# Optimization experiments

Hardware: AMD Instinct MI355X
Metric: run time of the kernel (lower is better)

The kernel has to match this reference:

```python
import jax, jax.numpy as jnp
import numpy as np
import math

B, N, M, H = 4, 1024, 1024, 512
EPS = 1e-5


def _ln(x, g, b):
    m = jnp.mean(x, axis=-1, keepdims=True)
    v = jnp.mean((x - m) ** 2, axis=-1, keepdims=True)
    return (x - m) * jax.lax.rsqrt(v + EPS) * g + b


def _heads(x, h):
    b, s, Hh = x.shape
    return x.reshape(b, s, h, Hh // h).transpose(0, 2, 1, 3)  # [b,h,s,d]


def _merge(x):
    b, h, s, d = x.shape
    return x.transpose(0, 2, 1, 3).reshape(b, s, h * d)


def _sdpa(q, k, v):
    d = q.shape[-1]
    a = jax.nn.softmax(jnp.einsum('bhqd,bhkd->bhqk', q, k) / math.sqrt(d), axis=-1)
    return jnp.einsum('bhqk,bhkd->bhqd', a, v)


def _attn(key, value, query, Wk, Wv, Wq, Wf, bf, g, b, h):
    residual = query
    K = _heads(key @ Wk, h)
    V = _heads(value @ Wv, h)
    Q = _heads(query @ Wq, h)
    r = _merge(_sdpa(Q, K, V))
    r = jnp.concatenate([residual, r], axis=-1) @ Wf + bf
    return _ln(r + residual, g, b)


def _sc_attn(x, x2, Wk, Wv, Wq, Wf, bf, g, b, h=2):
    residual = x
    sK, sV, sQ = _heads(x @ Wk, h), _heads(x @ Wv, h), _heads(x @ Wq, h)
    cK, cV, cQ = _heads(x2 @ Wk, h), _heads(x2 @ Wv, h), _heads(x2 @ Wq, h)
    r = _sdpa(sQ, sK, sV) + _sdpa(cQ, cK, cV) + _sdpa(cQ, sK, sV) + _sdpa(sQ, cK, cV)
    r = _merge(r)
    r = jnp.concatenate([residual, r], axis=-1) @ Wf + bf
    return _ln(r + residual, g, b)


def _forward(context_x, context_y, target_x, in_W, in_b, cx_W, cx_b, tx_W, tx_b,
             sc_Wk, sc_Wv, sc_Wq, sc_Wf, sc_bf, sc_g, sc_b,
             ca_Wk, ca_Wv, ca_Wq, ca_Wf, ca_bf, ca_g, ca_b):
    bsz = context_x.shape[0]
    y = context_y.reshape(bsz, -1, 4, 2)
    proj = lambda yd: jnp.concatenate([context_x, yd], axis=-1) @ in_W + in_b
    e = proj(y[:, :, 0, :])
    e1 = proj(y[:, :, 1, :])
    e2 = proj(y[:, :, 2, :])
    e3 = proj(y[:, :, 3, :])
    # first self pass: key2/value2/query2 == current encoder_input
    for i in range(2):
        e = _sc_attn(e, e, sc_Wk[i], sc_Wv[i], sc_Wq[i], sc_Wf[i], sc_bf[i], sc_g[i], sc_b[i])
    for x2 in (e1, e2, e3):
        for i in range(2):
            e = _sc_attn(e, x2, sc_Wk[i], sc_Wv[i], sc_Wq[i], sc_Wf[i], sc_bf[i], sc_g[i], sc_b[i])
    q = target_x @ tx_W + tx_b
    k = context_x @ cx_W + cx_b
    for i in range(2):
        q = _attn(k, e, q, ca_Wk[i], ca_Wv[i], ca_Wq[i], ca_Wf[i], ca_bf[i], ca_g[i], ca_b[i], h=4)
    return q


def setup_inputs() -> dict:
    key = jax.random.key(0)
    ks = jax.random.split(key, 24)
    w = lambda i, shape, s: jax.random.normal(ks[i], shape, jnp.float32) * s
    return {
        'context_x': jax.random.normal(ks[0], (B, N, 1), jnp.float32),
        'context_y': jax.random.normal(ks[1], (B, N, 8), jnp.float32),
        'target_x': jax.random.normal(ks[2], (B, M, 1), jnp.float32),
        'in_W': w(3, (3, H), 0.5), 'in_b': jnp.zeros((H,), jnp.float32),
        'cx_W': w(4, (1, H), 0.5), 'cx_b': jnp.zeros((H,), jnp.float32),
        'tx_W': w(5, (1, H), 0.5), 'tx_b': jnp.zeros((H,), jnp.float32),
        'sc_Wk': w(6, (2, H, H), 0.03), 'sc_Wv': w(7, (2, H, H), 0.03), 'sc_Wq': w(8, (2, H, H), 0.03),
        'sc_Wf': w(9, (2, 2 * H, H), 0.03), 'sc_bf': jnp.zeros((2, H), jnp.float32),
        'sc_g': jnp.ones((2, H), jnp.float32), 'sc_b': jnp.zeros((2, H), jnp.float32),
        'ca_Wk': w(10, (2, H, H), 0.03), 'ca_Wv': w(11, (2, H, H), 0.03), 'ca_Wq': w(12, (2, H, H), 0.03),
        'ca_Wf': w(13, (2, 2 * H, H), 0.03), 'ca_bf': jnp.zeros((2, H), jnp.float32),
        'ca_g': jnp.ones((2, H), jnp.float32), 'ca_b': jnp.zeros((2, H), jnp.float32),
    }


def reference(context_x, context_y, target_x, in_W, in_b, cx_W, cx_b, tx_W, tx_b,
              sc_Wk, sc_Wv, sc_Wq, sc_Wf, sc_bf, sc_g, sc_b,
              ca_Wk, ca_Wv, ca_Wq, ca_Wf, ca_bf, ca_g, ca_b):
    return _forward(context_x, context_y, target_x, in_W, in_b, cx_W, cx_b, tx_W, tx_b,
                    sc_Wk, sc_Wv, sc_Wq, sc_Wf, sc_bf, sc_g, sc_b,
                    ca_Wk, ca_Wv, ca_Wq, ca_Wf, ca_bf, ca_g, ca_b)
```

## Files before the change

kernel.cpp:

```cpp
#include <hip/hip_runtime.h>

#define DEVINL __device__ __forceinline__

typedef short bf16x8 __attribute__((ext_vector_type(8)));
typedef float f32x4 __attribute__((ext_vector_type(4)));

DEVINL unsigned f2b(float f) {
  unsigned u = __float_as_uint(f);
  u = (u + 0x7FFFu + ((u >> 16) & 1u)) >> 16;
  return u & 0xFFFFu;
}
DEVINL uint4 pack8(const float* v) {
  uint4 u;
  u.x = f2b(v[0]) | (f2b(v[1]) << 16);
  u.y = f2b(v[2]) | (f2b(v[3]) << 16);
  u.z = f2b(v[4]) | (f2b(v[5]) << 16);
  u.w = f2b(v[6]) | (f2b(v[7]) << 16);
  return u;
}

DEVINL float4 block_sum4(float4 v, float4* sh) {
  const int lane = threadIdx.x & 63, wid = threadIdx.x >> 6;
#pragma unroll
  for (int o = 32; o; o >>= 1) {
    v.x += __shfl_down(v.x, o);
    v.y += __shfl_down(v.y, o);
    v.z += __shfl_down(v.z, o);
    v.w += __shfl_down(v.w, o);
  }
  __syncthreads();
  if (lane == 0) sh[wid] = v;
  __syncthreads();
  float4 a = sh[0], b = sh[1], c = sh[2], d = sh[3], r;
  r.x = a.x + b.x + c.x + d.x;
  r.y = a.y + b.y + c.y + d.y;
  r.z = a.z + b.z + c.z + d.z;
  r.w = a.w + b.w + c.w + d.w;
  return r;
}
DEVINL float block_sum1(float v, float* sh) {
  const int lane = threadIdx.x & 63, wid = threadIdx.x >> 6;
#pragma unroll
  for (int o = 32; o; o >>= 1) v += __shfl_down(v, o);
  __syncthreads();
  if (lane == 0) sh[wid] = v;
  __syncthreads();
  return sh[0] + sh[1] + sh[2] + sh[3];
}

__global__ __launch_bounds__(256) void tabproj_kernel(
    const float* __restrict__ V, const float* __restrict__ bias,
    const float* __restrict__ W, float* __restrict__ P, int nvec, float scl) {
  __shared__ float4 sh4[4];
  const int j = blockIdx.x, tid = threadIdx.x;
  float acc[4] = {0.f, 0.f, 0.f, 0.f};
  for (int kk = tid; kk < 512; kk += 256) {
    const float w = W[(size_t)kk * 512 + j];
    for (int v = 0; v < nvec; ++v) acc[v] += V[(size_t)v * 512 + kk] * w;
    acc[3] += bias[kk] * w;
  }
  float4 packed = make_float4(acc[0], acc[1], acc[2], acc[3]);
  packed = block_sum4(packed, sh4);
  if (tid == 0) {
    const float vals[4] = {packed.x * scl, packed.y * scl, packed.z * scl, packed.w * scl};
    for (int v = 0; v < nvec; ++v) P[(size_t)v * 512 + j] = vals[v];
    P[(size_t)nvec * 512 + j] = vals[3];
  }
}

__global__ __launch_bounds__(256) void transpose_bf_kernel(
    const float* __restrict__ src, unsigned short* __restrict__ dst, int K, int N,
    float scl) {
  __shared__ float tile[32][33];
  const int n0 = blockIdx.x * 32, k0 = blockIdx.y * 32;
  const int tx = threadIdx.x, ty = threadIdx.y;
#pragma unroll
  for (int r = 0; r < 4; ++r)
    tile[ty + 8 * r][tx] = src[(size_t)(k0 + ty + 8 * r) * N + n0 + tx];
  __syncthreads();
#pragma unroll
  for (int r = 0; r < 4; ++r)
    dst[(size_t)(n0 + ty + 8 * r) * K + k0 + tx] =
        (unsigned short)f2b(scl * tile[tx][ty + 8 * r]);
}

__global__ __launch_bounds__(256) void vtrans_frag_kernel(
    const float* __restrict__ V, int ld, int nh, int D,
    unsigned short* __restrict__ Vfr) {
  __shared__ float tile[32][33];
  const int s0 = blockIdx.x * 32, d0 = blockIdx.y * 32;
  const int bh = blockIdx.z;
  const int b = bh / nh, h = bh % nh;
  const int tx = threadIdx.x, ty = threadIdx.y;
  const float* src = V + ((size_t)b * 1024 + s0) * ld + h * D + d0;
#pragma unroll
  for (int r = 0; r < 4; ++r)
    tile[ty + 8 * r][tx] = src[(size_t)(ty + 8 * r) * ld + tx];
  __syncthreads();
  const int idx = ty * 32 + tx;
  if (idx < 128) {
    const int dj = idx & 31, sch = idx >> 5;
    float v[8];
#pragma unroll
    for (int jj = 0; jj < 8; ++jj) v[jj] = tile[sch * 8 + jj][dj];
    const uint4 u = pack8(v);
    const int sc = s0 >> 5;
    const int dtile = (d0 + dj) >> 4;
    const int lane = sch * 16 + (dj & 15);
    *(uint4*)(Vfr + ((size_t)(bh * 32 + sc) * (D / 16) + dtile) * 512 + lane * 8) = u;
  }
}

__global__ __launch_bounds__(256) void affine3_pack_kernel(
    const float* __restrict__ cx, const float* __restrict__ cy, int sel,
    const float* __restrict__ TK, const float* __restrict__ TV,
    const float* __restrict__ TQ, unsigned short* __restrict__ Kfr,
    unsigned short* __restrict__ Qbf, float* __restrict__ Vf) {
  const int row = blockIdx.x;
  const int b = row >> 10, s = row & 1023;
  const float x = cx[row];
  const float* y = cy + (size_t)row * 8 + 2 * sel;
  const float y0 = y[0], y1 = y[1];
  const int t = threadIdx.x;
  if (t < 128) {
    const bool isQ = t >= 64;
    const int c = t & 63;
    const int h = c >> 5;
    const int d0 = (c & 31) * 8;
    const float* T = isQ ? TQ : TK;
    float v[8];
#pragma unroll
    for (int j = 0; j < 8; ++j) {
      const int col = h * 256 + d0 + j;
      v[j] = x * T[col] + y0 * T[512 + col] + y1 * T[1024 + col] + T[1536 + col];
    }
    const uint4 u = pack8(v);
    const int bh = b * 2 + h;
    if (isQ) {
      *(uint4*)(Qbf + ((size_t)bh * 1024 + s) * 256 + d0) = u;
    } else {
      const int kc = d0 >> 5;
      const int lane = ((d0 & 31) >> 3) * 16 + (s & 15);
      *(uint4*)(Kfr + ((size_t)(bh * 8 + kc) * 64 + (s >> 4)) * 512 + lane * 8) = u;
    }
  } else {
    const int col0 = (t - 128) * 4;
    float4 o;
    float* op = (float*)&o;
#pragma unroll
    for (int j = 0; j < 4; ++j) {
      const int col = col0 + j;
      op[j] = x * TV[col] + y0 * TV[512 + col] + y1 * TV[1024 + col] + TV[1536 + col];
    }
    *(float4*)(Vf + (size_t)row * 512 + col0) = o;
  }
}

__global__ __launch_bounds__(64) void rank1_pack_kernel(
    const float* __restrict__ x, const float* __restrict__ T,
    unsigned short* __restrict__ dst, int isQ) {
  const int row = blockIdx.x;
  const int b = row >> 10, s = row & 1023;
  const float xv = x[row];
  const int c = threadIdx.x;
  const int h = c >> 4;
  const int d0 = (c & 15) * 8;
  float v[8];
#pragma unroll
  for (int j = 0; j < 8; ++j) {
    const int col = h * 128 + d0 + j;
    v[j] = xv * T[col] + T[512 + col];
  }
  const uint4 u = pack8(v);
  const int bh = b * 4 + h;
  if (isQ) {
    *(uint4*)(dst + ((size_t)bh * 1024 + s) * 128 + d0) = u;
  } else {
    const int kc = d0 >> 5;
    const int lane = ((d0 & 31) >> 3) * 16 + (s & 15);
    *(uint4*)(dst + ((size_t)(bh * 4 + kc) * 64 + (s >> 4)) * 512 + lane * 8) = u;
  }
}

__global__ __launch_bounds__(512) void affine3_kernel(
    const float* __restrict__ cx, const float* __restrict__ cy, int sel,
    const float* __restrict__ W3, const float* __restrict__ bias,
    float* __restrict__ out, unsigned short* __restrict__ outb) {
  const int r = blockIdx.x, j = threadIdx.x;
  const float* y = cy + (size_t)r * 8 + 2 * sel;
  const float v = cx[r] * W3[j] + y[0] * W3[512 + j] + y[1] * W3[1024 + j] + bias[j];
  if (out) out[(size_t)r * 512 + j] = v;
  if (outb) outb[(size_t)r * 512 + j] = (unsigned short)f2b(v);
}

__global__ __launch_bounds__(512) void rank1_kernel(
    const float* __restrict__ x, const float* __restrict__ w,
    const float* __restrict__ b, float* __restrict__ out,
    unsigned short* __restrict__ outb) {
  const int r = blockIdx.x, j = threadIdx.x;
  const float v = x[r] * w[j] + b[j];
  if (out) out[(size_t)r * 512 + j] = v;
  if (outb) outb[(size_t)r * 512 + j] = (unsigned short)f2b(v);
}

__global__ __launch_bounds__(256) void gemm_mfma_kernel(
    const unsigned short* __restrict__ A0, int K0,
    const unsigned short* __restrict__ A1, int K1,
    const unsigned short* __restrict__ Wt, const float* __restrict__ bias,
    float* __restrict__ C, int M, int N) {
  constexpr int BM = 128, BN = 64, BK = 32, LDP = 40;
  __shared__ unsigned short As[2][BM * LDP];
  __shared__ unsigned short Bs[2][BN * LDP];
  const int tid = threadIdx.x;
  const int lane = tid & 63, w = tid >> 6;
  const int bm = blockIdx.y * BM, bn = blockIdx.x * BN;
  const int wm = (w & 1) * 64, wn = (w >> 1) * 32;
  const int l15 = lane & 15, lq = lane >> 4;
  const int ar = tid >> 1, ac = (tid & 1) * 16;
  const int br = tid >> 2, bc = (tid & 3) * 8;
  const int Ktot = K0 + K1;
  f32x4 acc[4][2] = {};
  uint4 ra0, ra1, rb0;
#define GLOAD(k0_)                                                         \
  do {                                                                     \
    const unsigned short* A_;                                              \
    int kk_, Ak_;                                                          \
    if ((k0_) < K0) { A_ = A0; kk_ = (k0_); Ak_ = K0; }                    \
    else            { A_ = A1; kk_ = (k0_) - K0; Ak_ = K1; }               \
    ra0 = *(const uint4*)(A_ + (size_t)(bm + ar) * Ak_ + kk_ + ac);        \
    ra1 = *(const uint4*)(A_ + (size_t)(bm + ar) * Ak_ + kk_ + ac + 8);    \
    rb0 = *(const uint4*)(Wt + (size_t)(bn + br) * Ktot + (k0_) + bc);     \
  } while (0)
  GLOAD(0);
  *(uint4*)(As[0] + ar * LDP + ac) = ra0;
  *(uint4*)(As[0] + ar * LDP + ac + 8) = ra1;
  *(uint4*)(Bs[0] + br * LDP + bc) = rb0;
  __syncthreads();
  int buf = 0;
  for (int k0 = 0; k0 < Ktot; k0 += BK) {
    const bool more = (k0 + BK) < Ktot;
    if (more) GLOAD(k0 + BK);
    bf16x8 af[4], bfr[2];
#pragma unroll
    for (int mt = 0; mt < 4; ++mt)
      af[mt] = *(const bf16x8*)(As[buf] + (wm + mt * 16 + l15) * LDP + lq * 8);
#pragma unroll
    for (int nt = 0; nt < 2; ++nt)
      bfr[nt] = *(const bf16x8*)(Bs[buf] + (wn + nt * 16 + l15) * LDP + lq * 8);
#pragma unroll
    for (int mt = 0; mt < 4; ++mt)
#pragma unroll
      for (int nt = 0; nt < 2; ++nt)
        acc[mt][nt] =
            __builtin_amdgcn_mfma_f32_16x16x32_bf16(af[mt], bfr[nt], acc[mt][nt], 0, 0, 0);
    if (more) {
      *(uint4*)(As[buf ^ 1] + ar * LDP + ac) = ra0;
      *(uint4*)(As[buf ^ 1] + ar * LDP + ac + 8) = ra1;
      *(uint4*)(Bs[buf ^ 1] + br * LDP + bc) = rb0;
    }
    __syncthreads();
    buf ^= 1;
  }
#undef GLOAD
#pragma unroll
  for (int nt = 0; nt < 2; ++nt) {
    const int col = bn + wn + nt * 16 + l15;
    const float bv = bias ? bias[col] : 0.f;
#pragma unroll
    for (int mt = 0; mt < 4; ++mt) {
#pragma unroll
      for (int r = 0; r < 4; ++r) {
        const int row = bm + wm + mt * 16 + lq * 4 + r;
        C[(size_t)row * N + col] = acc[mt][nt][r] + bv;
      }
    }
  }
}

template <int MODE>
__global__ __launch_bounds__(256) void gemm_pack_kernel(
    const unsigned short* __restrict__ A0, const unsigned short* __restrict__ Wt,
    unsigned short* __restrict__ Kfr, unsigned short* __restrict__ Vfr,
    unsigned short* __restrict__ Qbf) {
  constexpr int BM = 128, BN = 64, BK = 32, LDP = 40, K = 512;
  __shared__ unsigned short As[2][BM * LDP];
  __shared__ unsigned short Bs[2][BN * LDP];
  const int tid = threadIdx.x;
  const int lane = tid & 63, w = tid >> 6;
  const int bm = blockIdx.y * BM, bn = blockIdx.x * BN;
  const int wm = (w & 1) * 64, wn = (w >> 1) * 32;
  const int l15 = lane & 15, lq = lane >> 4;
  const int ar = tid >> 1, ac = (tid & 1) * 16;
  const int br = tid >> 2, bc = (tid & 3) * 8;
  f32x4 acc[4][2] = {};
  uint4 ra0 = *(const uint4*)(A0 + (size_t)(bm + ar) * K + ac);
  uint4 ra1 = *(const uint4*)(A0 + (size_t)(bm + ar) * K + ac + 8);
  uint4 rb0 = *(const uint4*)(Wt + (size_t)(bn + br) * K + bc);
  *(uint4*)(As[0] + ar * LDP + ac) = ra0;
  *(uint4*)(As[0] + ar * LDP + ac + 8) = ra1;
  *(uint4*)(Bs[0] + br * LDP + bc) = rb0;
  __syncthreads();
  int buf = 0;
  for (int k0 = 0; k0 < K; k0 += BK) {
    const bool more = (k0 + BK) < K;
    if (more) {
      ra0 = *(const uint4*)(A0 + (size_t)(bm + ar) * K + k0 + BK + ac);
      ra1 = *(const uint4*)(A0 + (size_t)(bm + ar) * K + k0 + BK + ac + 8);
      rb0 = *(const uint4*)(Wt + (size_t)(bn + br) * K + k0 + BK + bc);
    }
    bf16x8 af[4], bfr[2];
#pragma unroll
    for (int mt = 0; mt < 4; ++mt)
      af[mt] = *(const bf16x8*)(As[buf] + (wm + mt * 16 + l15) * LDP + lq * 8);
#pragma unroll
    for (int nt = 0; nt < 2; ++nt)
      bfr[nt] = *(const bf16x8*)(Bs[buf] + (wn + nt * 16 + l15) * LDP + lq * 8);
#pragma unroll
    for (int mt = 0; mt < 4; ++mt)
#pragma unroll
      for (int nt = 0; nt < 2; ++nt)
        acc[mt][nt] =
            __builtin_amdgcn_mfma_f32_16x16x32_bf16(af[mt], bfr[nt], acc[mt][nt], 0, 0, 0);
    if (more) {
      *(uint4*)(As[buf ^ 1] + ar * LDP + ac) = ra0;
      *(uint4*)(As[buf ^ 1] + ar * LDP + ac + 8) = ra1;
      *(uint4*)(Bs[buf ^ 1] + br * LDP + bc) = rb0;
    }
    __syncthreads();
    buf ^= 1;
  }
  const int b = bm >> 10;
  const int s0base = (bm & 1023) + wm + lq * 4;
#pragma unroll
  for (int nt = 0; nt < 2; ++nt) {
    const int col = bn + wn + nt * 16 + l15;
    int sec, h, d, nh2, Dv;
    if constexpr (MODE == 0) {
      sec = col >> 9; const int c = col & 511; h = c >> 8; d = c & 255; nh2 = 2; Dv = 256;
    } else if constexpr (MODE == 1) {
      sec = 1; h = col >> 7; d = col & 127; nh2 = 4; Dv = 128;
    } else {
      sec = 2; h = col >> 7; d = col & 127; nh2 = 4; Dv = 128;
    }
    const int bh = b * nh2 + h;
#pragma unroll
    for (int mt = 0; mt < 4; ++mt) {
      const int s0 = s0base + mt * 16;
      const float* a = (const float*)&acc[mt][nt];
      if (sec == 2) {
        unsigned short* q = Qbf + ((size_t)bh * 1024 + s0) * Dv + d;
#pragma unroll
        for (int r = 0; r < 4; ++r) q[(size_t)r * Dv] = (unsigned short)f2b(a[r]);
      } else if (sec == 0) {
        unsigned short* kp = Kfr +
            ((size_t)(bh * 8 + (d >> 5)) * 64 + (s0 >> 4)) * 512 +
            ((d & 31) >> 3) * 128 + (d & 7);
#pragma unroll
        for (int r = 0; r < 4; ++r)
          kp[((s0 & 15) + r) * 8] = (unsigned short)f2b(a[r]);
      } else {
        unsigned short* vp = Vfr +
            ((size_t)(bh * 32 + (s0 >> 5)) * (Dv / 16) + (d >> 4)) * 512 +
            (((s0 >> 3) & 3) * 16 + (d & 15)) * 8 + (s0 & 7);
        uint2 u;
        u.x = f2b(a[0]) | (f2b(a[1]) << 16);
        u.y = f2b(a[2]) | (f2b(a[3]) << 16);
        *(uint2*)vp = u;
      }
    }
  }
}

template <int D, int NKV>
__global__ __launch_bounds__(256, 2) void attn_mfma_kernel(
    const unsigned short* __restrict__ Qa, const unsigned short* __restrict__ Qb,
    const unsigned short* __restrict__ KfrA, const unsigned short* __restrict__ KfrB,
    const unsigned short* __restrict__ VfrA, const unsigned short* __restrict__ VfrB,
    float post_scale, int nh, unsigned short* __restrict__ R,
    float* __restrict__ Rp) {
  constexpr int NQS = NKV;
  constexpr int QP = D + 8;
  constexpr int WP = 1024 + 8;
  constexpr int DT = D / 64;
  const int tid = threadIdx.x;
  const int lane = tid & 63, w = tid >> 6;
  const int l15 = lane & 15, lq = lane >> 4;
  const int nbh = 4 * nh;
  int bx = blockIdx.x;
  int side = 0;
  if constexpr (NKV == 2) { side = bx >> 9; bx &= 511; }
  const int bh = bx % nbh;
  const int qb16 = (bx / nbh) * 16;
  const int b = bh / nh, head = bh % nh;
  const size_t rowb = (size_t)b * 1024;
  const int colo = head * D;

  __shared__ unsigned short qsh[NQS * 16 * QP];
  __shared__ unsigned short wsh[16 * WP];
  __shared__ float redA[4][16];
  __shared__ float redB[4][16];

  for (int idx = tid; idx < NQS * 16 * (D / 8); idx += 256) {
    const int st = idx / (16 * (D / 8));
    const int rem = idx - st * 16 * (D / 8);
    const int r = rem / (D / 8), ch = rem - r * (D / 8);
    const unsigned short* Q = st ? Qb : Qa;
    const uint4 u = *(const uint4*)(Q + ((size_t)bh * 1024 + qb16 + r) * D + ch * 8);
    *(uint4*)(qsh + st * 16 * QP + r * QP + ch * 8) = u;
  }
  __syncthreads();

  const unsigned short* Kp = (side ? KfrB : KfrA) + (size_t)bh * ((size_t)D * 1024);
  const unsigned short* Vp = (side ? VfrB : VfrA) + (size_t)bh * ((size_t)D * 1024);

  f32x4 acc[NQS][16] = {};
#pragma unroll 1
  for (int kc = 0; kc < D / 32; ++kc) {
    bf16x8 kf[16];
#pragma unroll
    for (int st = 0; st < 16; ++st)
      kf[st] = *(const bf16x8*)(Kp + ((size_t)kc * 64 + w * 16 + st) * 512 + lane * 8);
    const bf16x8 qa = *(const bf16x8*)(qsh + l15 * QP + kc * 32 + lq * 8);
    __builtin_amdgcn_s_setprio(1);
#pragma unroll
    for (int st = 0; st < 16; ++st)
      acc[0][st] = __builtin_amdgcn_mfma_f32_16x16x32_bf16(qa, kf[st], acc[0][st], 0, 0, 0);
    __builtin_amdgcn_s_setprio(0);
    if constexpr (NQS == 2) {
      const bf16x8 qb2 = *(const bf16x8*)(qsh + 16 * QP + l15 * QP + kc * 32 + lq * 8);
      __builtin_amdgcn_s_setprio(1);
#pragma unroll
      for (int st = 0; st < 16; ++st)
        acc[1][st] =
            __builtin_amdgcn_mfma_f32_16x16x32_bf16(qb2, kf[st], acc[1][st], 0, 0, 0);
      __builtin_amdgcn_s_setprio(0);
    }
  }

  float psA[4] = {0.f, 0.f, 0.f, 0.f}, psB[4] = {0.f, 0.f, 0.f, 0.f};
#pragma unroll
  for (int st = 0; st < 16; ++st)
#pragma unroll
    for (int r = 0; r < 4; ++r) {
      acc[0][st][r] = __expf(acc[0][st][r]);
      psA[r] += acc[0][st][r];
      if constexpr (NQS == 2) {
        acc[1][st][r] = __expf(acc[1][st][r]);
        psB[r] += acc[1][st][r];
      }
    }
#pragma unroll
  for (int o = 1; o < 16; o <<= 1)
#pragma unroll
    for (int r = 0; r < 4; ++r) {
      psA[r] += __shfl_xor(psA[r], o);
      if constexpr (NQS == 2) psB[r] += __shfl_xor(psB[r], o);
    }
  if (l15 == 0) {
#pragma unroll
    for (int r = 0; r < 4; ++r) {
      redA[w][lq * 4 + r] = psA[r];
      if constexpr (NQS == 2) redB[w][lq * 4 + r] = psB[r];
    }
  }
  __syncthreads();
  float invA[4], invB[4];
#pragma unroll
  for (int r = 0; r < 4; ++r) {
    invA[r] = 1.f / (redA[0][lq * 4 + r] + redA[1][lq * 4 + r] +
                     redA[2][lq * 4 + r] + redA[3][lq * 4 + r]);
    if constexpr (NQS == 2)
      invB[r] = 1.f / (redB[0][lq * 4 + r] + redB[1][lq * 4 + r] +
                       redB[2][lq * 4 + r] + redB[3][lq * 4 + r]);
  }
#pragma unroll
  for (int st = 0; st < 16; ++st)
#pragma unroll
    for (int r = 0; r < 4; ++r) {
      float wv = acc[0][st][r] * invA[r];
      if constexpr (NQS == 2) wv += acc[1][st][r] * invB[r];
      wsh[(lq * 4 + r) * WP + w * 256 + st * 16 + l15] = (unsigned short)f2b(wv);
    }
  __syncthreads();

  f32x4 acc_o[DT] = {};
#pragma unroll 1
  for (int sc = 0; sc < 32; sc += 2) {
    bf16x8 pa[2], vb[2][DT];
#pragma unroll
    for (int u = 0; u < 2; ++u) {
      pa[u] = *(const bf16x8*)(wsh + l15 * WP + (sc + u) * 32 + lq * 8);
#pragma unroll
      for (int dt = 0; dt < DT; ++dt)
        vb[u][dt] = *(const bf16x8*)(
            Vp + ((size_t)(sc + u) * (D / 16) + w * DT + dt) * 512 + lane * 8);
    }
    __builtin_amdgcn_s_setprio(1);
#pragma unroll
    for (int u = 0; u < 2; ++u)
#pragma unroll
      for (int dt = 0; dt < DT; ++dt)
        acc_o[dt] =
            __builtin_amdgcn_mfma_f32_16x16x32_bf16(pa[u], vb[u][dt], acc_o[dt], 0, 0, 0);
    __builtin_amdgcn_s_setprio(0);
  }

  if constexpr (NKV == 2) {
    float* dst = Rp + (size_t)side * (4096 * 512) + (rowb + qb16) * 512 + colo;
#pragma unroll
    for (int dt = 0; dt < DT; ++dt)
#pragma unroll
      for (int r = 0; r < 4; ++r) {
        const int q = lq * 4 + r;
        const int d = w * (DT * 16) + dt * 16 + l15;
        dst[(size_t)q * 512 + d] = acc_o[dt][r];
      }
  } else {
#pragma unroll
    for (int dt = 0; dt < DT; ++dt)
#pragma unroll
      for (int r = 0; r < 4; ++r) {
        const int q = lq * 4 + r;
        const int d = w * (DT * 16) + dt * 16 + l15;
        R[(rowb + qb16 + q) * 512 + colo + d] =
            (unsigned short)f2b(acc_o[dt][r] * post_scale);
      }
  }
}

__global__ __launch_bounds__(256) void addcvt_kernel(
    const float* __restrict__ A, const float* __restrict__ B,
    unsigned short* __restrict__ O) {
  const size_t i = ((size_t)blockIdx.x * 256 + threadIdx.x) * 8;
  float v[8];
  *(float4*)v = *(const float4*)(A + i);
  *(float4*)(v + 4) = *(const float4*)(A + i + 4);
  const float4 b0 = *(const float4*)(B + i);
  const float4 b1 = *(const float4*)(B + i + 4);
  v[0] += b0.x; v[1] += b0.y; v[2] += b0.z; v[3] += b0.w;
  v[4] += b1.x; v[5] += b1.y; v[6] += b1.z; v[7] += b1.w;
  *(uint4*)(O + i) = pack8(v);
}

__global__ __launch_bounds__(256) void ln_kernel(
    const float* __restrict__ G, const float* __restrict__ res,
    const float* __restrict__ g, const float* __restrict__ b,
    float* __restrict__ out, unsigned short* __restrict__ outb) {
  __shared__ float sh[4];
  const int row = blockIdx.x, tid = threadIdx.x;
  const size_t off = (size_t)row * 512;
  const float x0 = G[off + tid] + res[off + tid];
  const float x1 = G[off + tid + 256] + res[off + tid + 256];
  const float mean = block_sum1(x0 + x1, sh) * (1.0f / 512.0f);
  const float d0 = x0 - mean, d1 = x1 - mean;
  const float var = block_sum1(d0 * d0 + d1 * d1, sh) * (1.0f / 512.0f);
  const float inv = rsqrtf(var + 1e-5f);
  const float y0 = d0 * inv * g[tid] + b[tid];
  const float y1 = d1 * inv * g[tid + 256] + b[tid + 256];
  out[off + tid] = y0;
  out[off + tid + 256] = y1;
  if (outb) {
    outb[off + tid] = (unsigned short)f2b(y0);
    outb[off + tid + 256] = (unsigned short)f2b(y1);
  }
}

extern "C" void kernel_launch(void* const* d_in, const int* in_sizes, int n_in,
                              void* d_out, int out_size, void* d_ws, size_t ws_size,
                              hipStream_t stream) {
  typedef unsigned short ushort_t;
  const float* cx   = (const float*)d_in[0];
  const float* cy   = (const float*)d_in[1];
  const float* txp  = (const float*)d_in[2];
  const float* in_W = (const float*)d_in[3];
  const float* in_b = (const float*)d_in[4];
  const float* cx_W = (const float*)d_in[5];
  const float* cx_b = (const float*)d_in[6];
  const float* tx_W = (const float*)d_in[7];
  const float* tx_b = (const float*)d_in[8];
  const float* sWk  = (const float*)d_in[9];
  const float* sWv  = (const float*)d_in[10];
  const float* sWq  = (const float*)d_in[11];
  const float* sWf  = (const float*)d_in[12];
  const float* sbf  = (const float*)d_in[13];
  const float* sg   = (const float*)d_in[14];
  const float* sb   = (const float*)d_in[15];
  const float* aWk  = (const float*)d_in[16];
  const float* aWv  = (const float*)d_in[17];
  const float* aWq  = (const float*)d_in[18];
  const float* aWf  = (const float*)d_in[19];
  const float* abf  = (const float*)d_in[20];
  const float* ag   = (const float*)d_in[21];
  const float* ab   = (const float*)d_in[22];

  const float SSC = 0.0625f;
  const float CSC = 0.08838834764831845f;

  const size_t MB = 1024 * 1024;
  char* ws = (char*)d_ws;
  float*    E     = (float*)(ws + 0 * MB);
  ushort_t* Ebf   = (ushort_t*)(ws + 8 * MB);
  float*    QA    = (float*)(ws + 12 * MB);
  ushort_t* QAbf  = (ushort_t*)(ws + 20 * MB);
  ushort_t* Rbbf  = (ushort_t*)(ws + 24 * MB);
  float*    G     = (float*)(ws + 28 * MB);
  float*    Rp    = G;
  ushort_t* KfrA  = (ushort_t*)(ws + 52 * MB);
  ushort_t* VfrA  = (ushort_t*)(ws + 56 * MB);
  ushort_t* QbfA  = (ushort_t*)(ws + 60 * MB);
  ushort_t* KfrB  = (ushort_t*)(ws + 64 * MB);
  ushort_t* VfrB  = (ushort_t*)(ws + 68 * MB);
  ushort_t* QbfB  = (ushort_t*)(ws + 72 * MB);
  float*    cVf   = (float*)(ws + 76 * MB);
  ushort_t* Wkvqt[2] = {(ushort_t*)(ws + 92 * MB),
                        (ushort_t*)(ws + 92 * MB + 1536 * 1024)};
  ushort_t* Wft[2]   = {(ushort_t*)(ws + 95 * MB), (ushort_t*)(ws + 96 * MB)};
  ushort_t* aWvt[2]  = {(ushort_t*)(ws + 97 * MB),
                        (ushort_t*)(ws + 97 * MB + 512 * 1024)};
  ushort_t* aWqt1    = (ushort_t*)(ws + 98 * MB);
  ushort_t* aWft[2]  = {(ushort_t*)(ws + 99 * MB), (ushort_t*)(ws + 100 * MB)};
  float*    Ttab     = (float*)(ws + 101 * MB);

  float* T_sc[2][3];
  for (int i = 0; i < 2; ++i)
    for (int w = 0; w < 3; ++w) T_sc[i][w] = Ttab + (size_t)(i * 3 + w) * 2048;
  float* T_cak[2] = {Ttab + 12288, Ttab + 12288 + 1024};
  float* T_caq0 = Ttab + 14336;

  const dim3 tb(32, 8);
  const dim3 tg512(16, 16), tg1024(16, 32);

  for (int i = 0; i < 2; ++i) {
    transpose_bf_kernel<<<tg512, tb, 0, stream>>>(sWk + (size_t)i * 262144, Wkvqt[i], 512, 512, 1.f);
    transpose_bf_kernel<<<tg512, tb, 0, stream>>>(sWv + (size_t)i * 262144, Wkvqt[i] + 512 * 512, 512, 512, 1.f);
    transpose_bf_kernel<<<tg512, tb, 0, stream>>>(sWq + (size_t)i * 262144, Wkvqt[i] + 1024 * 512, 512, 512, SSC);
    transpose_bf_kernel<<<tg1024, tb, 0, stream>>>(sWf + (size_t)i * 524288, Wft[i], 1024, 512, 1.f);
    transpose_bf_kernel<<<tg512, tb, 0, stream>>>(aWv + (size_t)i * 262144, aWvt[i], 512, 512, 1.f);
    transpose_bf_kernel<<<tg1024, tb, 0, stream>>>(aWf + (size_t)i * 524288, aWft[i], 1024, 512, 1.f);
    tabproj_kernel<<<512, 256, 0, stream>>>(in_W, in_b, sWk + (size_t)i * 262144, T_sc[i][0], 3, 1.f);
    tabproj_kernel<<<512, 256, 0, stream>>>(in_W, in_b, sWv + (size_t)i * 262144, T_sc[i][1], 3, 1.f);
    tabproj_kernel<<<512, 256, 0, stream>>>(in_W, in_b, sWq + (size_t)i * 262144, T_sc[i][2], 3, SSC);
    tabproj_kernel<<<512, 256, 0, stream>>>(cx_W, cx_b, aWk + (size_t)i * 262144, T_cak[i], 1, 1.f);
  }
  transpose_bf_kernel<<<tg512, tb, 0, stream>>>(aWq + 262144, aWqt1, 512, 512, CSC);
  tabproj_kernel<<<512, 256, 0, stream>>>(tx_W, tx_b, aWq, T_caq0, 1, CSC);

  affine3_kernel<<<4096, 512, 0, stream>>>(cx, cy, 0, in_W, in_b, E, Ebf);
  rank1_kernel<<<4096, 512, 0, stream>>>(txp, tx_W, tx_b, QA, QAbf);

  for (int p = 0; p < 4; ++p) {
    for (int i = 0; i < 2; ++i) {
      gemm_pack_kernel<0><<<dim3(24, 32), 256, 0, stream>>>(Ebf, Wkvqt[i], KfrA, VfrA,
                                                            QbfA);
      if (p > 0) {
        affine3_pack_kernel<<<4096, 256, 0, stream>>>(cx, cy, p, T_sc[i][0], T_sc[i][1],
                                                      T_sc[i][2], KfrB, QbfB, cVf);
        vtrans_frag_kernel<<<dim3(32, 8, 8), tb, 0, stream>>>(cVf, 512, 2, 256, VfrB);
        attn_mfma_kernel<256, 2><<<1024, 256, 0, stream>>>(
            QbfA, QbfB, KfrA, KfrB, VfrA, VfrB, 1.0f, 2, nullptr, Rp);
        addcvt_kernel<<<1024, 256, 0, stream>>>(Rp, Rp + 4096 * 512, Rbbf);
      } else {
        attn_mfma_kernel<256, 1><<<512, 256, 0, stream>>>(
            QbfA, QbfA, KfrA, KfrA, VfrA, VfrA, 4.0f, 2, Rbbf, nullptr);
      }
      gemm_mfma_kernel<<<dim3(8, 32), 256, 0, stream>>>(Ebf, 512, Rbbf, 512, Wft[i],
                                                        sbf + (size_t)i * 512, G, 4096, 512);
      ln_kernel<<<4096, 256, 0, stream>>>(G, E, sg + (size_t)i * 512, sb + (size_t)i * 512,
                                          E, Ebf);
    }
  }

  for (int i = 0; i < 2; ++i) {
    rank1_pack_kernel<<<4096, 64, 0, stream>>>(cx, T_cak[i], KfrA, 0);
    gemm_pack_kernel<1><<<dim3(8, 32), 256, 0, stream>>>(Ebf, aWvt[i], nullptr, VfrA,
                                                         nullptr);
    if (i == 0) {
      rank1_pack_kernel<<<4096, 64, 0, stream>>>(txp, T_caq0, QbfB, 1);
    } else {
      gemm_pack_kernel<2><<<dim3(8, 32), 256, 0, stream>>>(QAbf, aWqt1, nullptr, nullptr,
                                                           QbfB);
    }
    attn_mfma_kernel<128, 1><<<1024, 256, 0, stream>>>(
        QbfB, QbfB, KfrA, KfrA, VfrA, VfrA, 1.0f, 4, Rbbf, nullptr);
    gemm_mfma_kernel<<<dim3(8, 32), 256, 0, stream>>>(QAbf, 512, Rbbf, 512, aWft[i],
                                                      abf + (size_t)i * 512, G, 4096, 512);
    ln_kernel<<<4096, 256, 0, stream>>>(G, QA, ag + (size_t)i * 512, ab + (size_t)i * 512,
                                        (i == 1) ? (float*)d_out : QA,
                                        (i == 1) ? nullptr : QAbf);
  }
  (void)in_sizes; (void)n_in; (void)out_size; (void)ws_size;
}
```

Baseline: 1.087 ms.

## Split-K Wf GEMM, fuse partial-sum add into GEMM and LN, batch weight prep

The output-projection GEMM is split along K into two z-slices, one for the residual half and one for the attention half. Each slice writes its own partial result, and the layernorm sums the two partials. This doubles the number of blocks in a 256-block GEMM to improve occupancy on the many CUs. The separate addcvt kernel is removed: the two fp32 attention partials are summed and converted to bf16 inside the GEMM's A-load. Weight transposes and table projections are batched into three launches instead of about 26. The cost is extra fp32 traffic for the second partial buffer and a heavier A-load path.

```diff
diff --git a/kernel.cpp b/kernel.cpp
--- a/kernel.cpp
+++ b/kernel.cpp
@@ -48,9 +48,34 @@
   return sh[0] + sh[1] + sh[2] + sh[3];
 }
 
-__global__ __launch_bounds__(256) void tabproj_kernel(
-    const float* __restrict__ V, const float* __restrict__ bias,
-    const float* __restrict__ W, float* __restrict__ P, int nvec, float scl) {
+__global__ __launch_bounds__(256) void tabproj9_kernel(
+    const float* __restrict__ in_W, const float* __restrict__ in_b,
+    const float* __restrict__ cx_W, const float* __restrict__ cx_b,
+    const float* __restrict__ tx_W, const float* __restrict__ tx_b,
+    const float* __restrict__ sWk, const float* __restrict__ sWv,
+    const float* __restrict__ sWq, const float* __restrict__ aWk,
+    const float* __restrict__ aWq, float* __restrict__ Ttab) {
+  const int z = blockIdx.y;
+  const float* V;
+  const float* bias;
+  const float* W;
+  float* P;
+  int nvec;
+  float scl = 1.f;
+  if (z < 6) {
+    V = in_W; bias = in_b; nvec = 3;
+    const int i = z / 3, wsel = z % 3;
+    W = (wsel == 0 ? sWk : wsel == 1 ? sWv : sWq) + (size_t)i * 262144;
+    P = Ttab + (size_t)z * 2048;
+    if (wsel == 2) scl = 0.0625f;
+  } else if (z < 8) {
+    V = cx_W; bias = cx_b; nvec = 1;
+    W = aWk + (size_t)(z - 6) * 262144;
+    P = Ttab + 12288 + (size_t)(z - 6) * 1024;
+  } else {
+    V = tx_W; bias = tx_b; nvec = 1;
+    W = aWq; P = Ttab + 14336; scl = 0.08838834764831845f;
+  }
   __shared__ float4 sh4[4];
   const int j = blockIdx.x, tid = threadIdx.x;
   float acc[4] = {0.f, 0.f, 0.f, 0.f};
@@ -68,20 +93,57 @@
   }
 }
 
-__global__ __launch_bounds__(256) void transpose_bf_kernel(
-    const float* __restrict__ src, unsigned short* __restrict__ dst, int K, int N,
-    float scl) {
+__global__ __launch_bounds__(256) void transpose_kvq_kernel(
+    const float* __restrict__ sWk, const float* __restrict__ sWv,
+    const float* __restrict__ sWq, const float* __restrict__ aWv,
+    const float* __restrict__ aWq, unsigned short* __restrict__ Wkvqt0,
+    unsigned short* __restrict__ aWvt0, unsigned short* __restrict__ aWqt1) {
+  const int z = blockIdx.z;
+  const float* src;
+  unsigned short* dst;
+  float scl = 1.f;
+  if (z < 6) {
+    const int i = z / 3, wsel = z % 3;
+    src = (wsel == 0 ? sWk : wsel == 1 ? sWv : sWq) + (size_t)i * 262144;
+    dst = Wkvqt0 + (size_t)i * 786432 + (size_t)wsel * 262144;
+    if (wsel == 2) scl = 0.0625f;
+  } else if (z < 8) {
+    src = aWv + (size_t)(z - 6) * 262144;
+    dst = aWvt0 + (size_t)(z - 6) * 262144;
+  } else {
+    src = aWq + 262144; dst = aWqt1; scl = 0.08838834764831845f;
+  }
   __shared__ float tile[32][33];
   const int n0 = blockIdx.x * 32, k0 = blockIdx.y * 32;
   const int tx = threadIdx.x, ty = threadIdx.y;
 #pragma unroll
   for (int r = 0; r < 4; ++r)
-    tile[ty + 8 * r][tx] = src[(size_t)(k0 + ty + 8 * r) * N + n0 + tx];
+    tile[ty + 8 * r][tx] = src[(size_t)(k0 + ty + 8 * r) * 512 + n0 + tx];
   __syncthreads();
 #pragma unroll
   for (int r = 0; r < 4; ++r)
-    dst[(size_t)(n0 + ty + 8 * r) * K + k0 + tx] =
+    dst[(size_t)(n0 + ty + 8 * r) * 512 + k0 + tx] =
         (unsigned short)f2b(scl * tile[tx][ty + 8 * r]);
+}
+
+__global__ __launch_bounds__(256) void transpose_f_kernel(
+    const float* __restrict__ sWf, const float* __restrict__ aWf,
+    unsigned short* __restrict__ Wft0, unsigned short* __restrict__ aWft0) {
+  const int z = blockIdx.z;
+  const float* src = (z < 2 ? sWf + (size_t)z * 524288 : aWf + (size_t)(z - 2) * 524288);
+  unsigned short* dst =
+      (z < 2 ? Wft0 + (size_t)z * 524288 : aWft0 + (size_t)(z - 2) * 524288);
+  __shared__ float tile[32][33];
+  const int n0 = blockIdx.x * 32, k0 = blockIdx.y * 32;
+  const int tx = threadIdx.x, ty = threadIdx.y;
+#pragma unroll
+  for (int r = 0; r < 4; ++r)
+    tile[ty + 8 * r][tx] = src[(size_t)(k0 + ty + 8 * r) * 512 + n0 + tx];
+  __syncthreads();
+#pragma unroll
+  for (int r = 0; r < 4; ++r)
+    dst[(size_t)(n0 + ty + 8 * r) * 1024 + k0 + tx] =
+        (unsigned short)f2b(tile[tx][ty + 8 * r]);
 }
 
 __global__ __launch_bounds__(256) void vtrans_frag_kernel(
@@ -203,14 +265,15 @@
   if (outb) outb[(size_t)r * 512 + j] = (unsigned short)f2b(v);
 }
 
-__global__ __launch_bounds__(256) void gemm_mfma_kernel(
-    const unsigned short* __restrict__ A0, int K0,
-    const unsigned short* __restrict__ A1, int K1,
+__global__ __launch_bounds__(256) void gemm_wf_kernel(
+    const unsigned short* __restrict__ A0, const unsigned short* __restrict__ A1,
+    const float* __restrict__ F0, const float* __restrict__ F1,
     const unsigned short* __restrict__ Wt, const float* __restrict__ bias,
-    float* __restrict__ C, int M, int N) {
-  constexpr int BM = 128, BN = 64, BK = 32, LDP = 40;
+    float* __restrict__ C0, float* __restrict__ C1) {
+  constexpr int BM = 128, BN = 64, BK = 32, LDP = 40, K = 512, N = 512;
   __shared__ unsigned short As[2][BM * LDP];
   __shared__ unsigned short Bs[2][BN * LDP];
+  const int kz = blockIdx.z;
   const int tid = threadIdx.x;
   const int lane = tid & 63, w = tid >> 6;
   const int bm = blockIdx.y * BM, bn = blockIdx.x * BN;
@@ -218,18 +281,32 @@
   const int l15 = lane & 15, lq = lane >> 4;
   const int ar = tid >> 1, ac = (tid & 1) * 16;
   const int br = tid >> 2, bc = (tid & 3) * 8;
-  const int Ktot = K0 + K1;
+  const unsigned short* A = kz ? A1 : A0;
+  const bool useF = (kz != 0) && (F0 != nullptr);
+  const size_t arow = (size_t)(bm + ar) * 512;
+  const size_t brow = (size_t)(bn + br) * 1024 + (size_t)kz * 512;
   f32x4 acc[4][2] = {};
   uint4 ra0, ra1, rb0;
-#define GLOAD(k0_)                                                         \
-  do {                                                                     \
-    const unsigned short* A_;                                              \
-    int kk_, Ak_;                                                          \
-    if ((k0_) < K0) { A_ = A0; kk_ = (k0_); Ak_ = K0; }                    \
-    else            { A_ = A1; kk_ = (k0_) - K0; Ak_ = K1; }               \
-    ra0 = *(const uint4*)(A_ + (size_t)(bm + ar) * Ak_ + kk_ + ac);        \
-    ra1 = *(const uint4*)(A_ + (size_t)(bm + ar) * Ak_ + kk_ + ac + 8);    \
-    rb0 = *(const uint4*)(Wt + (size_t)(bn + br) * Ktot + (k0_) + bc);     \
+#define GLOAD(k0_)                                                          \
+  do {                                                                      \
+    if (useF) {                                                             \
+      const float* p0 = F0 + arow + (k0_) + ac;                             \
+      const float* p1 = F1 + arow + (k0_) + ac;                             \
+      float s[16];                                                          \
+      const float4 x0 = *(const float4*)p0, x1 = *(const float4*)(p0 + 4);  \
+      const float4 x2 = *(const float4*)(p0 + 8), x3 = *(const float4*)(p0 + 12); \
+      const float4 y0 = *(const float4*)p1, y1 = *(const float4*)(p1 + 4);  \
+      const float4 y2 = *(const float4*)(p1 + 8), y3 = *(const float4*)(p1 + 12); \
+      s[0] = x0.x + y0.x; s[1] = x0.y + y0.y; s[2] = x0.z + y0.z; s[3] = x0.w + y0.w; \
+      s[4] = x1.x + y1.x; s[5] = x1.y + y1.y; s[6] = x1.z + y1.z; s[7] = x1.w + y1.w; \
+      s[8] = x2.x + y2.x; s[9] = x2.y + y2.y; s[10] = x2.z + y2.z; s[11] = x2.w + y2.w; \
+      s[12] = x3.x + y3.x; s[13] = x3.y + y3.y; s[14] = x3.z + y3.z; s[15] = x3.w + y3.w; \
+      ra0 = pack8(s); ra1 = pack8(s + 8);                                   \
+    } else {                                                                \
+      ra0 = *(const uint4*)(A + arow + (k0_) + ac);                         \
+      ra1 = *(const uint4*)(A + arow + (k0_) + ac + 8);                     \
+    }                                                                       \
+    rb0 = *(const uint4*)(Wt + brow + (k0_) + bc);                          \
   } while (0)
   GLOAD(0);
   *(uint4*)(As[0] + ar * LDP + ac) = ra0;
@@ -237,8 +314,8 @@
   *(uint4*)(Bs[0] + br * LDP + bc) = rb0;
   __syncthreads();
   int buf = 0;
-  for (int k0 = 0; k0 < Ktot; k0 += BK) {
-    const bool more = (k0 + BK) < Ktot;
+  for (int k0 = 0; k0 < K; k0 += BK) {
+    const bool more = (k0 + BK) < K;
     if (more) GLOAD(k0 + BK);
     bf16x8 af[4], bfr[2];
 #pragma unroll
@@ -262,10 +339,11 @@
     buf ^= 1;
   }
 #undef GLOAD
+  float* C = kz ? C1 : C0;
 #pragma unroll
   for (int nt = 0; nt < 2; ++nt) {
     const int col = bn + wn + nt * 16 + l15;
-    const float bv = bias ? bias[col] : 0.f;
+    const float bv = (kz && bias) ? bias[col] : 0.f;
 #pragma unroll
     for (int mt = 0; mt < 4; ++mt) {
 #pragma unroll
@@ -528,29 +606,16 @@
   }
 }
 
-__global__ __launch_bounds__(256) void addcvt_kernel(
-    const float* __restrict__ A, const float* __restrict__ B,
-    unsigned short* __restrict__ O) {
-  const size_t i = ((size_t)blockIdx.x * 256 + threadIdx.x) * 8;
-  float v[8];
-  *(float4*)v = *(const float4*)(A + i);
-  *(float4*)(v + 4) = *(const float4*)(A + i + 4);
-  const float4 b0 = *(const float4*)(B + i);
-  const float4 b1 = *(const float4*)(B + i + 4);
-  v[0] += b0.x; v[1] += b0.y; v[2] += b0.z; v[3] += b0.w;
-  v[4] += b1.x; v[5] += b1.y; v[6] += b1.z; v[7] += b1.w;
-  *(uint4*)(O + i) = pack8(v);
-}
-
 __global__ __launch_bounds__(256) void ln_kernel(
-    const float* __restrict__ G, const float* __restrict__ res,
-    const float* __restrict__ g, const float* __restrict__ b,
-    float* __restrict__ out, unsigned short* __restrict__ outb) {
+    const float* __restrict__ G0, const float* __restrict__ G1,
+    const float* __restrict__ res, const float* __restrict__ g,
+    const float* __restrict__ b, float* __restrict__ out,
+    unsigned short* __restrict__ outb) {
   __shared__ float sh[4];
   const int row = blockIdx.x, tid = threadIdx.x;
   const size_t off = (size_t)row * 512;
-  const float x0 = G[off + tid] + res[off + tid];
-  const float x1 = G[off + tid + 256] + res[off + tid + 256];
+  const float x0 = G0[off + tid] + G1[off + tid] + res[off + tid];
+  const float x1 = G0[off + tid + 256] + G1[off + tid + 256] + res[off + tid + 256];
   const float mean = block_sum1(x0 + x1, sh) * (1.0f / 512.0f);
   const float d0 = x0 - mean, d1 = x1 - mean;
   const float var = block_sum1(d0 * d0 + d1 * d1, sh) * (1.0f / 512.0f);
@@ -593,9 +658,6 @@
   const float* ag   = (const float*)d_in[21];
   const float* ab   = (const float*)d_in[22];
 
-  const float SSC = 0.0625f;
-  const float CSC = 0.08838834764831845f;
-
   const size_t MB = 1024 * 1024;
   char* ws = (char*)d_ws;
   float*    E     = (float*)(ws + 0 * MB);
@@ -603,8 +665,8 @@
   float*    QA    = (float*)(ws + 12 * MB);
   ushort_t* QAbf  = (ushort_t*)(ws + 20 * MB);
   ushort_t* Rbbf  = (ushort_t*)(ws + 24 * MB);
-  float*    G     = (float*)(ws + 28 * MB);
-  float*    Rp    = G;
+  float*    Rp    = (float*)(ws + 28 * MB);
+  float*    G0    = (float*)(ws + 44 * MB);
   ushort_t* KfrA  = (ushort_t*)(ws + 52 * MB);
   ushort_t* VfrA  = (ushort_t*)(ws + 56 * MB);
   ushort_t* QbfA  = (ushort_t*)(ws + 60 * MB);
@@ -612,14 +674,17 @@
   ushort_t* VfrB  = (ushort_t*)(ws + 68 * MB);
   ushort_t* QbfB  = (ushort_t*)(ws + 72 * MB);
   float*    cVf   = (float*)(ws + 76 * MB);
-  ushort_t* Wkvqt[2] = {(ushort_t*)(ws + 92 * MB),
-                        (ushort_t*)(ws + 92 * MB + 1536 * 1024)};
-  ushort_t* Wft[2]   = {(ushort_t*)(ws + 95 * MB), (ushort_t*)(ws + 96 * MB)};
-  ushort_t* aWvt[2]  = {(ushort_t*)(ws + 97 * MB),
-                        (ushort_t*)(ws + 97 * MB + 512 * 1024)};
-  ushort_t* aWqt1    = (ushort_t*)(ws + 98 * MB);
-  ushort_t* aWft[2]  = {(ushort_t*)(ws + 99 * MB), (ushort_t*)(ws + 100 * MB)};
-  float*    Ttab     = (float*)(ws + 101 * MB);
+  float*    G1    = (float*)(ws + 84 * MB);
+  ushort_t* Wkvqt0 = (ushort_t*)(ws + 92 * MB);
+  ushort_t* Wkvqt[2] = {Wkvqt0, Wkvqt0 + 786432};
+  ushort_t* Wft0   = (ushort_t*)(ws + 95 * MB);
+  ushort_t* Wft[2] = {Wft0, Wft0 + 524288};
+  ushort_t* aWvt0  = (ushort_t*)(ws + 97 * MB);
+  ushort_t* aWvt[2] = {aWvt0, aWvt0 + 262144};
+  ushort_t* aWqt1  = (ushort_t*)(ws + 98 * MB);
+  ushort_t* aWft0  = (ushort_t*)(ws + 99 * MB);
+  ushort_t* aWft[2] = {aWft0, aWft0 + 524288};
+  float*    Ttab   = (float*)(ws + 101 * MB);
 
   float* T_sc[2][3];
   for (int i = 0; i < 2; ++i)
@@ -628,22 +693,12 @@
   float* T_caq0 = Ttab + 14336;
 
   const dim3 tb(32, 8);
-  const dim3 tg512(16, 16), tg1024(16, 32);
-
-  for (int i = 0; i < 2; ++i) {
-    transpose_bf_kernel<<<tg512, tb, 0, stream>>>(sWk + (size_t)i * 262144, Wkvqt[i], 512, 512, 1.f);
-    transpose_bf_kernel<<<tg512, tb, 0, stream>>>(sWv + (size_t)i * 262144, Wkvqt[i] + 512 * 512, 512, 512, 1.f);
-    transpose_bf_kernel<<<tg512, tb, 0, stream>>>(sWq + (size_t)i * 262144, Wkvqt[i] + 1024 * 512, 512, 512, SSC);
-    transpose_bf_kernel<<<tg1024, tb, 0, stream>>>(sWf + (size_t)i * 524288, Wft[i], 1024, 512, 1.f);
-    transpose_bf_kernel<<<tg512, tb, 0, stream>>>(aWv + (size_t)i * 262144, aWvt[i], 512, 512, 1.f);
-    transpose_bf_kernel<<<tg1024, tb, 0, stream>>>(aWf + (size_t)i * 524288, aWft[i], 1024, 512, 1.f);
-    tabproj_kernel<<<512, 256, 0, stream>>>(in_W, in_b, sWk + (size_t)i * 262144, T_sc[i][0], 3, 1.f);
-    tabproj_kernel<<<512, 256, 0, stream>>>(in_W, in_b, sWv + (size_t)i * 262144, T_sc[i][1], 3, 1.f);
-    tabproj_kernel<<<512, 256, 0, stream>>>(in_W, in_b, sWq + (size_t)i * 262144, T_sc[i][2], 3, SSC);
-    tabproj_kernel<<<512, 256, 0, stream>>>(cx_W, cx_b, aWk + (size_t)i * 262144, T_cak[i], 1, 1.f);
-  }
-  transpose_bf_kernel<<<tg512, tb, 0, stream>>>(aWq + 262144, aWqt1, 512, 512, CSC);
-  tabproj_kernel<<<512, 256, 0, stream>>>(tx_W, tx_b, aWq, T_caq0, 1, CSC);
+
+  transpose_kvq_kernel<<<dim3(16, 16, 9), tb, 0, stream>>>(sWk, sWv, sWq, aWv, aWq,
+                                                           Wkvqt0, aWvt0, aWqt1);
+  transpose_f_kernel<<<dim3(16, 32, 4), tb, 0, stream>>>(sWf, aWf, Wft0, aWft0);
+  tabproj9_kernel<<<dim3(512, 9), 256, 0, stream>>>(in_W, in_b, cx_W, cx_b, tx_W, tx_b,
+                                                    sWk, sWv, sWq, aWk, aWq, Ttab);
 
   affine3_kernel<<<4096, 512, 0, stream>>>(cx, cy, 0, in_W, in_b, E, Ebf);
   rank1_kernel<<<4096, 512, 0, stream>>>(txp, tx_W, tx_b, QA, QAbf);
@@ -652,21 +707,23 @@
     for (int i = 0; i < 2; ++i) {
       gemm_pack_kernel<0><<<dim3(24, 32), 256, 0, stream>>>(Ebf, Wkvqt[i], KfrA, VfrA,
                                                             QbfA);
+      const float* F0 = nullptr;
+      const float* F1 = nullptr;
       if (p > 0) {
         affine3_pack_kernel<<<4096, 256, 0, stream>>>(cx, cy, p, T_sc[i][0], T_sc[i][1],
                                                       T_sc[i][2], KfrB, QbfB, cVf);
         vtrans_frag_kernel<<<dim3(32, 8, 8), tb, 0, stream>>>(cVf, 512, 2, 256, VfrB);
         attn_mfma_kernel<256, 2><<<1024, 256, 0, stream>>>(
             QbfA, QbfB, KfrA, KfrB, VfrA, VfrB, 1.0f, 2, nullptr, Rp);
-        addcvt_kernel<<<1024, 256, 0, stream>>>(Rp, Rp + 4096 * 512, Rbbf);
+        F0 = Rp; F1 = Rp + 4096 * 512;
       } else {
         attn_mfma_kernel<256, 1><<<512, 256, 0, stream>>>(
             QbfA, QbfA, KfrA, KfrA, VfrA, VfrA, 4.0f, 2, Rbbf, nullptr);
       }
-      gemm_mfma_kernel<<<dim3(8, 32), 256, 0, stream>>>(Ebf, 512, Rbbf, 512, Wft[i],
-                                                        sbf + (size_t)i * 512, G, 4096, 512);
-      ln_kernel<<<4096, 256, 0, stream>>>(G, E, sg + (size_t)i * 512, sb + (size_t)i * 512,
-                                          E, Ebf);
+      gemm_wf_kernel<<<dim3(8, 32, 2), 256, 0, stream>>>(
+          Ebf, Rbbf, F0, F1, Wft[i], sbf + (size_t)i * 512, G0, G1);
+      ln_kernel<<<4096, 256, 0, stream>>>(G0, G1, E, sg + (size_t)i * 512,
+                                          sb + (size_t)i * 512, E, Ebf);
     }
   }
 
@@ -682,9 +739,10 @@
     }
     attn_mfma_kernel<128, 1><<<1024, 256, 0, stream>>>(
         QbfB, QbfB, KfrA, KfrA, VfrA, VfrA, 1.0f, 4, Rbbf, nullptr);
-    gemm_mfma_kernel<<<dim3(8, 32), 256, 0, stream>>>(QAbf, 512, Rbbf, 512, aWft[i],
-                                                      abf + (size_t)i * 512, G, 4096, 512);
-    ln_kernel<<<4096, 256, 0, stream>>>(G, QA, ag + (size_t)i * 512, ab + (size_t)i * 512,
+    gemm_wf_kernel<<<dim3(8, 32, 2), 256, 0, stream>>>(
+        QAbf, Rbbf, nullptr, nullptr, aWft[i], abf + (size_t)i * 512, G0, G1);
+    ln_kernel<<<4096, 256, 0, stream>>>(G0, G1, QA, ag + (size_t)i * 512,
+                                        ab + (size_t)i * 512,
                                         (i == 1) ? (float*)d_out : QA,
                                         (i == 1) ? nullptr : QAbf);
   }
```

Measured after the change: 1.060 ms. 1.03x faster.
